# Kernel optimization log

Hardware: AMD Instinct MI355X
Metric: run time of the kernel (lower is better)

Reference implementation:

```python
import jax, jax.numpy as jnp
import numpy as np

N = 50000        # nodes
DEG = 16         # avg degree
E_RAND = N * DEG # random directed edges (before self-loops)
B = 4
F_IN = 64
F_OUT = 64


def _build_normalized_adjacency():
    """COO form of A_hat = D^{-1/2} (A + I) D^{-1/2} for a random sparse graph."""
    rng = np.random.default_rng(0)
    src = rng.integers(0, N, size=E_RAND)
    dst = rng.integers(0, N, size=E_RAND)
    rows = np.concatenate([src, np.arange(N)])  # add self-loops (A + I)
    cols = np.concatenate([dst, np.arange(N)])
    d = np.bincount(rows, minlength=N).astype(np.float32)  # row sums of A_tilde
    d_inv_sqrt = np.where(d > 0, 1.0 / np.sqrt(d), 0.0).astype(np.float32)
    vals = d_inv_sqrt[rows] * d_inv_sqrt[cols]
    return rows.astype(np.int32), cols.astype(np.int32), vals


def setup_inputs() -> dict:
    key = jax.random.key(0)
    k1, k2 = jax.random.split(key, 2)
    rows, cols, vals = _build_normalized_adjacency()
    x = jax.random.normal(k1, (B, N, F_IN), dtype=jnp.float32)
    # trunc_normal_(std=0.1) approximated by scaled normal
    weight = jax.random.normal(k2, (F_IN, F_OUT), dtype=jnp.float32) * 0.1
    bias = jnp.full((F_OUT,), 0.1, dtype=jnp.float32)
    return {
        "x": x,
        "vals": jnp.asarray(vals),
        "weight": weight,
        "bias": bias,
        "rows": jnp.asarray(rows),
        "cols": jnp.asarray(cols),
    }


def reference(x, vals, weight, bias, rows, cols):
    # SpMM: agg[b, r, f] = sum_e vals[e] * x[b, cols[e], f], scattered to rows[e]
    contrib = x[:, cols, :] * vals[None, :, None]          # [B, E, F_in]
    agg = jax.ops.segment_sum(contrib.transpose(1, 0, 2),  # [E, B, F_in]
                              rows, num_segments=N)        # [N, B, F_in]
    agg = agg.transpose(1, 0, 2)                           # [B, N, F_in]
    out = jnp.einsum('bnf,fo->bno', agg, weight) + bias    # dense GEMM + bias
    return jax.nn.elu(out)
```

## Files before the change

### kernel.cpp

```cpp
#include <hip/hip_runtime.h>
#include <math.h>

#define NNODES 50000
#define BB 4
#define FF 64
#define CAP 64

#define TROWS 32
#define GEMM_NB ((BB * NNODES) / TROWS)
#define RPB 4


__device__ inline unsigned short f2bf(float f) {
    unsigned u = __float_as_uint(f);
    u += 0x7fffu + ((u >> 16) & 1u);
    return (unsigned short)(u >> 16);
}

__device__ inline void bf4fma(float v, uint2 hv, float& a0, float& a1, float& a2, float& a3) {
    a0 = fmaf(v, __uint_as_float(hv.x << 16),         a0);
    a1 = fmaf(v, __uint_as_float(hv.x & 0xffff0000u), a1);
    a2 = fmaf(v, __uint_as_float(hv.y << 16),         a2);
    a3 = fmaf(v, __uint_as_float(hv.y & 0xffff0000u), a3);
}


__global__ __launch_bounds__(256) void prep_kernel(const int* __restrict__ rows,
                                                   const int* __restrict__ cols,
                                                   const float* __restrict__ vals,
                                                   int* __restrict__ cnt,
                                                   unsigned* __restrict__ edata, int ES, int EPB,
                                                   int cstride,
                                                   const float* __restrict__ x,
                                                   const float* __restrict__ w,
                                                   unsigned short* __restrict__ h) {
    __shared__ float xs[TROWS][68];
    __shared__ float wsh[64][68];
    int t = threadIdx.x;
    long rowBase = (long)blockIdx.x * TROWS;

    #pragma unroll
    for (int i = 0; i < 2; ++i) {
        int s = t + i * 256;
        int r = s >> 4, c4 = s & 15;
        const float4* xp = (const float4*)(x + (rowBase + r) * 64 + c4 * 4);
        float4 xv;
        xv.x = __builtin_nontemporal_load(&xp->x);
        xv.y = __builtin_nontemporal_load(&xp->y);
        xv.z = __builtin_nontemporal_load(&xp->z);
        xv.w = __builtin_nontemporal_load(&xp->w);
        *(float4*)&xs[r][c4 * 4] = xv;
    }
    #pragma unroll
    for (int i = 0; i < 4; ++i) {
        int s = t + i * 256;
        int r = s >> 4, c4 = s & 15;
        *(float4*)&wsh[r][c4 * 4] = *(const float4*)(w + r * 64 + c4 * 4);
    }
    __syncthreads();

    int ty = t >> 4, tx = t & 15;
    int r0 = ty * 2, c0 = tx * 4;
    float acc[2][4] = {};
    #pragma unroll
    for (int f4 = 0; f4 < 16; ++f4) {
        float a[2][4], b[4][4];
        #pragma unroll
        for (int i = 0; i < 2; ++i)
            #pragma unroll
            for (int k = 0; k < 4; ++k) a[i][k] = xs[r0 + i][f4 * 4 + k];
        #pragma unroll
        for (int k = 0; k < 4; ++k)
            #pragma unroll
            for (int j = 0; j < 4; ++j) b[k][j] = wsh[f4 * 4 + k][c0 + j];
        #pragma unroll
        for (int i = 0; i < 2; ++i)
            #pragma unroll
            for (int k = 0; k < 4; ++k)
                #pragma unroll
                for (int j = 0; j < 4; ++j) acc[i][j] = fmaf(a[i][k], b[k][j], acc[i][j]);
    }
    #pragma unroll
    for (int i = 0; i < 2; ++i) {
        long m = rowBase + r0 + i;
        int  b = (int)(m / NNODES);
        int  n = (int)(m - (long)b * NNODES);
        ushort4 o;
        o.x = f2bf(acc[i][0]); o.y = f2bf(acc[i][1]);
        o.z = f2bf(acc[i][2]); o.w = f2bf(acc[i][3]);
        *(ushort4*)(h + ((size_t)n * BB + b) * 64 + c0) = o;
    }

    int e = blockIdx.x * EPB + t;
    if (t < EPB && e < ES) {
        int r = rows[e];
        int pos = atomicAdd(&cnt[(size_t)r * cstride], 1);
        if (pos < CAP) {
            unsigned p = ((unsigned)f2bf(vals[e]) << 16) | (unsigned)cols[e];
            edata[(size_t)r * CAP + pos] = p;
        }
    }
}


__global__ __launch_bounds__(256) void gather_kernel(const unsigned short* __restrict__ h,
                                                     const int* __restrict__ cnt,
                                                     const unsigned* __restrict__ edata,
                                                     const float* __restrict__ vals,
                                                     const float* __restrict__ bias,
                                                     float* __restrict__ out,
                                                     int cstride, int ES) {
    int wave = threadIdx.x >> 6;
    int lane = threadIdx.x & 63;
    int r = blockIdx.x * RPB + wave;
    if (r >= NNODES) return;
    int deg = cnt[(size_t)r * cstride];
    if (deg > CAP) deg = CAP;
    int b  = lane >> 4;
    int fq = lane & 15;
    const unsigned short* hb = h + b * 64 + fq * 4;
    unsigned my_p = 0u;
    if (lane < deg) {
        const unsigned* ep = &edata[(size_t)r * CAP + lane];
        my_p = __builtin_nontemporal_load(ep);
    }
    float vs = vals[ES + r];
    uint2 hs = *(const uint2*)(hb + (size_t)r * 256);
    float4 b4 = ((const float4*)bias)[fq];

    float a0 = 0.f, a1 = 0.f, a2 = 0.f, a3 = 0.f;
    int dg8 = (deg + 7) & ~7;
    for (int k = 0; k < dg8; k += 8) {
        unsigned p0 = __shfl(my_p, k,     64), p1 = __shfl(my_p, k + 1, 64);
        unsigned p2 = __shfl(my_p, k + 2, 64), p3 = __shfl(my_p, k + 3, 64);
        unsigned p4 = __shfl(my_p, k + 4, 64), p5 = __shfl(my_p, k + 5, 64);
        unsigned p6 = __shfl(my_p, k + 6, 64), p7 = __shfl(my_p, k + 7, 64);
        uint2 h0 = *(const uint2*)(hb + (size_t)(p0 & 0xFFFFu) * 256);
        uint2 h1 = *(const uint2*)(hb + (size_t)(p1 & 0xFFFFu) * 256);
        uint2 h2 = *(const uint2*)(hb + (size_t)(p2 & 0xFFFFu) * 256);
        uint2 h3 = *(const uint2*)(hb + (size_t)(p3 & 0xFFFFu) * 256);
        uint2 h4 = *(const uint2*)(hb + (size_t)(p4 & 0xFFFFu) * 256);
        uint2 h5 = *(const uint2*)(hb + (size_t)(p5 & 0xFFFFu) * 256);
        uint2 h6 = *(const uint2*)(hb + (size_t)(p6 & 0xFFFFu) * 256);
        uint2 h7 = *(const uint2*)(hb + (size_t)(p7 & 0xFFFFu) * 256);
        bf4fma(__uint_as_float(p0 & 0xFFFF0000u), h0, a0, a1, a2, a3);
        bf4fma(__uint_as_float(p1 & 0xFFFF0000u), h1, a0, a1, a2, a3);
        bf4fma(__uint_as_float(p2 & 0xFFFF0000u), h2, a0, a1, a2, a3);
        bf4fma(__uint_as_float(p3 & 0xFFFF0000u), h3, a0, a1, a2, a3);
        bf4fma(__uint_as_float(p4 & 0xFFFF0000u), h4, a0, a1, a2, a3);
        bf4fma(__uint_as_float(p5 & 0xFFFF0000u), h5, a0, a1, a2, a3);
        bf4fma(__uint_as_float(p6 & 0xFFFF0000u), h6, a0, a1, a2, a3);
        bf4fma(__uint_as_float(p7 & 0xFFFF0000u), h7, a0, a1, a2, a3);
    }
    bf4fma(vs, hs, a0, a1, a2, a3);
    a0 += b4.x; a1 += b4.y; a2 += b4.z; a3 += b4.w;
    a0 = a0 > 0.f ? a0 : expm1f(a0);
    a1 = a1 > 0.f ? a1 : expm1f(a1);
    a2 = a2 > 0.f ? a2 : expm1f(a2);
    a3 = a3 > 0.f ? a3 : expm1f(a3);
    float4 o = make_float4(a0, a1, a2, a3);
    *(float4*)(out + ((size_t)b * NNODES + r) * 64 + fq * 4) = o;
}


static inline size_t align256(size_t x) { return (x + 255) & ~(size_t)255; }

extern "C" void kernel_launch(void* const* d_in, const int* in_sizes, int n_in,
                              void* d_out, int out_size, void* d_ws, size_t ws_size,
                              hipStream_t stream) {
    const float* x    = (const float*)d_in[0];
    const float* vals = (const float*)d_in[1];
    const float* w    = (const float*)d_in[2];
    const float* bias = (const float*)d_in[3];
    const int*   rows = (const int*)d_in[4];
    const int*   cols = (const int*)d_in[5];
    float* out = (float*)d_out;
    const int E  = in_sizes[1];
    const int ES = E - NNODES;

    size_t h_b     = align256((size_t)BB * NNODES * FF * sizeof(unsigned short));
    size_t edata_b = align256((size_t)NNODES * CAP * sizeof(unsigned));
    int cstride = 16;
    if (h_b + edata_b + align256((size_t)NNODES * 16 * sizeof(int)) > ws_size) cstride = 1;

    char* ws = (char*)d_ws;
    size_t off = 0;
    unsigned short* h = (unsigned short*)(ws + off);  off += h_b;
    int* cnt = (int*)(ws + off);
    off += align256((size_t)NNODES * cstride * sizeof(int));
    unsigned* edata = (unsigned*)(ws + off);          off += edata_b;

    int EPB = (ES + GEMM_NB - 1) / GEMM_NB;

    hipMemsetAsync(cnt, 0, (size_t)NNODES * cstride * sizeof(int), stream);
    prep_kernel<<<GEMM_NB, 256, 0, stream>>>(rows, cols, vals, cnt, edata, ES, EPB, cstride, x, w, h);
    gather_kernel<<<(NNODES + RPB - 1) / RPB, 256, 0, stream>>>(h, cnt, edata, vals, bias, out, cstride, ES);
}
```

Measured before the change: 110.9 us.

## Use fp16 MFMA for dense transform and enlarge prep tiles to 64 rows

The per-block x·W product in the prep kernel now converts x and a transposed W to fp16 in shared memory and runs it on 16x16x32 MFMA instructions in place of scalar FMAs. Tile height doubles to 64 rows, which halves the block count, and the edge scatter now gives each block a full 256 edges. Edge loads are issued at kernel start so their latency overlaps the GEMM. The fp16 cast of x adds rounding error, and the bf16 output is now written as scattered 2-byte stores instead of 8-byte vectors.

```diff
diff --git a/kernel.cpp b/kernel.cpp
--- a/kernel.cpp
+++ b/kernel.cpp
@@ -6,9 +6,13 @@
 #define FF 64
 #define CAP 64
 
-#define TROWS 32
+#define TROWS 64
 #define GEMM_NB ((BB * NNODES) / TROWS)
 #define RPB 4
+
+typedef _Float16 f16;
+typedef __attribute__((ext_vector_type(8))) _Float16 f16x8;
+typedef __attribute__((ext_vector_type(4))) float f32x4;
 
 
 __device__ inline unsigned short f2bf(float f) {
@@ -29,18 +33,24 @@
                                                    const int* __restrict__ cols,
                                                    const float* __restrict__ vals,
                                                    int* __restrict__ cnt,
-                                                   unsigned* __restrict__ edata, int ES, int EPB,
+                                                   unsigned* __restrict__ edata, int ES,
                                                    int cstride,
                                                    const float* __restrict__ x,
                                                    const float* __restrict__ w,
                                                    unsigned short* __restrict__ h) {
-    __shared__ float xs[TROWS][68];
-    __shared__ float wsh[64][68];
+    __shared__ f16 xs[64][72];
+    __shared__ f16 wt[64][72];
     int t = threadIdx.x;
     long rowBase = (long)blockIdx.x * TROWS;
 
+    int e = blockIdx.x * 256 + t;
+    bool has_e = (e < ES);
+    int r_e = 0, c_e = 0;
+    float v_e = 0.f;
+    if (has_e) { r_e = rows[e]; c_e = cols[e]; v_e = vals[e]; }
+
     #pragma unroll
-    for (int i = 0; i < 2; ++i) {
+    for (int i = 0; i < 4; ++i) {
         int s = t + i * 256;
         int r = s >> 4, c4 = s & 15;
         const float4* xp = (const float4*)(x + (rowBase + r) * 64 + c4 * 4);
@@ -49,55 +59,48 @@
         xv.y = __builtin_nontemporal_load(&xp->y);
         xv.z = __builtin_nontemporal_load(&xp->z);
         xv.w = __builtin_nontemporal_load(&xp->w);
-        *(float4*)&xs[r][c4 * 4] = xv;
-    }
-    #pragma unroll
-    for (int i = 0; i < 4; ++i) {
-        int s = t + i * 256;
-        int r = s >> 4, c4 = s & 15;
-        *(float4*)&wsh[r][c4 * 4] = *(const float4*)(w + r * 64 + c4 * 4);
+        xs[r][c4 * 4 + 0] = (f16)xv.x;
+        xs[r][c4 * 4 + 1] = (f16)xv.y;
+        xs[r][c4 * 4 + 2] = (f16)xv.z;
+        xs[r][c4 * 4 + 3] = (f16)xv.w;
+        float4 wv = *(const float4*)(w + r * 64 + c4 * 4);
+        wt[c4 * 4 + 0][r] = (f16)wv.x;
+        wt[c4 * 4 + 1][r] = (f16)wv.y;
+        wt[c4 * 4 + 2][r] = (f16)wv.z;
+        wt[c4 * 4 + 3][r] = (f16)wv.w;
     }
     __syncthreads();
 
-    int ty = t >> 4, tx = t & 15;
-    int r0 = ty * 2, c0 = tx * 4;
-    float acc[2][4] = {};
+    int wid = t >> 6, l = t & 63;
+    int arow = (wid << 4) + (l & 15);
+    int kg   = (l >> 4) << 3;
+    f16x8 aLo = *(const f16x8*)&xs[arow][kg];
+    f16x8 aHi = *(const f16x8*)&xs[arow][32 + kg];
+    f32x4 acc[4] = {{0.f,0.f,0.f,0.f},{0.f,0.f,0.f,0.f},{0.f,0.f,0.f,0.f},{0.f,0.f,0.f,0.f}};
     #pragma unroll
-    for (int f4 = 0; f4 < 16; ++f4) {
-        float a[2][4], b[4][4];
-        #pragma unroll
-        for (int i = 0; i < 2; ++i)
-            #pragma unroll
-            for (int k = 0; k < 4; ++k) a[i][k] = xs[r0 + i][f4 * 4 + k];
-        #pragma unroll
-        for (int k = 0; k < 4; ++k)
-            #pragma unroll
-            for (int j = 0; j < 4; ++j) b[k][j] = wsh[f4 * 4 + k][c0 + j];
-        #pragma unroll
-        for (int i = 0; i < 2; ++i)
-            #pragma unroll
-            for (int k = 0; k < 4; ++k)
-                #pragma unroll
-                for (int j = 0; j < 4; ++j) acc[i][j] = fmaf(a[i][k], b[k][j], acc[i][j]);
+    for (int c = 0; c < 4; ++c) {
+        f16x8 bLo = *(const f16x8*)&wt[c * 16 + (l & 15)][kg];
+        f16x8 bHi = *(const f16x8*)&wt[c * 16 + (l & 15)][32 + kg];
+        acc[c] = __builtin_amdgcn_mfma_f32_16x16x32_f16(aLo, bLo, acc[c], 0, 0, 0);
+        acc[c] = __builtin_amdgcn_mfma_f32_16x16x32_f16(aHi, bHi, acc[c], 0, 0, 0);
     }
+
+    int mloc = (l >> 4) << 2, fcol = l & 15;
     #pragma unroll
-    for (int i = 0; i < 2; ++i) {
-        long m = rowBase + r0 + i;
+    for (int reg = 0; reg < 4; ++reg) {
+        long m = rowBase + (wid << 4) + mloc + reg;
         int  b = (int)(m / NNODES);
         int  n = (int)(m - (long)b * NNODES);
-        ushort4 o;
-        o.x = f2bf(acc[i][0]); o.y = f2bf(acc[i][1]);
-        o.z = f2bf(acc[i][2]); o.w = f2bf(acc[i][3]);
-        *(ushort4*)(h + ((size_t)n * BB + b) * 64 + c0) = o;
+        unsigned short* hp = h + ((size_t)n * BB + b) * 64 + fcol;
+        #pragma unroll
+        for (int c = 0; c < 4; ++c) hp[c * 16] = f2bf(acc[c][reg]);
     }
 
-    int e = blockIdx.x * EPB + t;
-    if (t < EPB && e < ES) {
-        int r = rows[e];
-        int pos = atomicAdd(&cnt[(size_t)r * cstride], 1);
+    if (has_e) {
+        int pos = atomicAdd(&cnt[(size_t)r_e * cstride], 1);
         if (pos < CAP) {
-            unsigned p = ((unsigned)f2bf(vals[e]) << 16) | (unsigned)cols[e];
-            edata[(size_t)r * CAP + pos] = p;
+            unsigned p = ((unsigned)f2bf(v_e) << 16) | (unsigned)c_e;
+            edata[(size_t)r_e * CAP + pos] = p;
         }
     }
 }
@@ -190,9 +193,7 @@
     off += align256((size_t)NNODES * cstride * sizeof(int));
     unsigned* edata = (unsigned*)(ws + off);          off += edata_b;
 
-    int EPB = (ES + GEMM_NB - 1) / GEMM_NB;
-
     hipMemsetAsync(cnt, 0, (size_t)NNODES * cstride * sizeof(int), stream);
-    prep_kernel<<<GEMM_NB, 256, 0, stream>>>(rows, cols, vals, cnt, edata, ES, EPB, cstride, x, w, h);
+    prep_kernel<<<GEMM_NB, 256, 0, stream>>>(rows, cols, vals, cnt, edata, ES, cstride, x, w, h);
     gather_kernel<<<(NNODES + RPB - 1) / RPB, 256, 0, stream>>>(h, cnt, edata, vals, bias, out, cstride, ES);
 }
```

New measurement: 133.2 us. 20.1% more time.
